# Kernel tuning notes

Hardware: AMD Instinct MI355X
Metric: run time of the kernel (lower is better)

Reference implementation:

```python
import jax, jax.numpy as jnp
import numpy as np

G, T, S, M = 1024, 200, 16, 4  # groups, timesteps, state_size, measure_size


def setup_inputs() -> dict:
    key = jax.random.key(0)
    ks = jax.random.split(key, 6)
    inp = jax.random.normal(ks[0], (G, T, M), dtype=jnp.float32)
    # near-identity transition (stable dynamics)
    F = jnp.eye(S, dtype=jnp.float32) + 0.01 * jax.random.normal(ks[1], (S, S), dtype=jnp.float32)
    qa = jax.random.normal(ks[2], (S, S), dtype=jnp.float32)
    Q = 0.01 * (qa @ qa.T) / S + 1e-3 * jnp.eye(S, dtype=jnp.float32)  # PSD process noise
    H = jax.random.normal(ks[3], (M, S), dtype=jnp.float32) / jnp.sqrt(jnp.float32(S))
    ra = jax.random.normal(ks[4], (M, M), dtype=jnp.float32)
    R = 0.1 * (ra @ ra.T) / M + 1e-2 * jnp.eye(M, dtype=jnp.float32)  # PSD measurement noise
    init_mean = jnp.zeros((G, S), dtype=jnp.float32)
    # block-diag initial state cov (identity per process block)
    init_cov = jnp.broadcast_to(jnp.eye(S, dtype=jnp.float32), (G, S, S)).copy()
    return {"input": inp, "F": F, "Q": Q, "H": H, "R": R,
            "init_mean": init_mean, "init_cov": init_cov}


def reference(input, F, Q, H, R, init_mean, init_cov):
    """Kalman filter: at t=0 emit the initial prediction; for t>0, update the
    previous prediction with obs[t-1] then predict forward (matches the torch
    loop). Returns one-step-ahead state means/covs and measurement means/covs."""

    def step(carry, obs):  # obs: [G, M] (measurement at t-1)
        mean, cov = carry  # [G,S], [G,S,S]
        # --- update: K = P H^T S^-1, S = H P H^T + R ---
        HP = jnp.einsum('ms,gsk->gmk', H, cov)            # [G,M,S]
        Smat = jnp.einsum('gmk,nk->gmn', HP, H) + R       # [G,M,M]
        K = jnp.swapaxes(jnp.linalg.solve(Smat, HP), 1, 2)  # [G,S,M]
        resid = obs - mean @ H.T                          # [G,M]
        mean_u = mean + jnp.einsum('gsm,gm->gs', K, resid)
        cov_u = cov - K @ HP                              # (I - K H) P
        # --- predict: F x, F P F^T + Q ---
        mean_p = mean_u @ F.T
        cov_p = jnp.einsum('ij,gjk,lk->gil', F, cov_u, F) + Q
        return (mean_p, cov_p), (mean_p, cov_p)

    obs_seq = jnp.swapaxes(input[:, :-1, :], 0, 1)  # [T-1, G, M]
    _, (means_t, covs_t) = jax.lax.scan(step, (init_mean, init_cov), obs_seq)

    means = jnp.concatenate([init_mean[None], means_t], axis=0)  # [T,G,S]
    covs = jnp.concatenate([init_cov[None], covs_t], axis=0)     # [T,G,S,S]

    # compute_measurement for every stored prediction: H x, H P H^T + R
    meas_means = jnp.einsum('tgs,ms->tgm', means, H)             # [T,G,M]
    HPc = jnp.einsum('ms,tgsk->tgmk', H, covs)
    meas_covs = jnp.einsum('tgmk,nk->tgmn', HPc, H) + R          # [T,G,M,M]

    return (jnp.swapaxes(means, 0, 1),       # [G,T,S]
            jnp.swapaxes(covs, 0, 1),        # [G,T,S,S]
            jnp.swapaxes(meas_means, 0, 1),  # [G,T,M]
            jnp.swapaxes(meas_covs, 0, 1))   # [G,T,M,M]
```

## Files before the change

### kernel.cpp

```cpp
#include <hip/hip_runtime.h>

#define NG 1024
#define NT 200
#define NS 16
#define NM 4

#define LDS_FENCE() asm volatile("" ::: "memory")

template<int CTRL>
__device__ __forceinline__ double dpp_mov_d(double x) {
    const int lo = __double2loint(x), hi = __double2hiint(x);
    const int plo = __builtin_amdgcn_update_dpp(lo, lo, CTRL, 0xF, 0xF, false);
    const int phi = __builtin_amdgcn_update_dpp(hi, hi, CTRL, 0xF, 0xF, false);
    return __hiloint2double(phi, plo);
}
__device__ __forceinline__ double row16_allreduce_d(double x) {
    x += dpp_mov_d<0xB1>(x);
    x += dpp_mov_d<0x4E>(x);
    x += dpp_mov_d<0x141>(x);
    x += dpp_mov_d<0x140>(x);
    return x;
}
__device__ __forceinline__ double partner16_d(double x, int odd) {
#if __has_builtin(__builtin_amdgcn_permlane16_swap)
    const unsigned lo = (unsigned)__double2loint(x), hi = (unsigned)__double2hiint(x);
    auto rl = __builtin_amdgcn_permlane16_swap(lo, lo, false, false);
    auto rh = __builtin_amdgcn_permlane16_swap(hi, hi, false, false);
    return __hiloint2double((int)(odd ? rh[0] : rh[1]),
                            (int)(odd ? rl[0] : rl[1]));
#else
    (void)odd; return __shfl_xor(x, 16, 64);
#endif
}
__device__ __forceinline__ double partner32_d(double x, int up) {
#if __has_builtin(__builtin_amdgcn_permlane32_swap)
    const unsigned lo = (unsigned)__double2loint(x), hi = (unsigned)__double2hiint(x);
    auto rl = __builtin_amdgcn_permlane32_swap(lo, lo, false, false);
    auto rh = __builtin_amdgcn_permlane32_swap(hi, hi, false, false);
    return __hiloint2double((int)(up ? rh[0] : rh[1]),
                            (int)(up ? rl[0] : rl[1]));
#else
    (void)up; return __shfl_xor(x, 32, 64);
#endif
}
__device__ __forceinline__ double quad_allreduce_d(double x, int q) {
    x += partner16_d(x, q & 1);
    x += partner32_d(x, (q >> 1) & 1);
    return x;
}

__global__ __launch_bounds__(256, 1)
void kalman_kernel(const float* __restrict__ input,
                   const float* __restrict__ Fm,
                   const float* __restrict__ Qm,
                   const float* __restrict__ Hm,
                   const float* __restrict__ Rm,
                   const float* __restrict__ init_mean,
                   const float* __restrict__ init_cov,
                   float* __restrict__ out)
{
    const int lane = threadIdx.x & 63;
    const int wid  = threadIdx.x >> 6;
    const int g    = (blockIdx.x << 2) + wid;
    const int c    = lane & 15;
    const int q    = lane >> 4;

    __shared__ __align__(16) float  lds3[4][NS][20];
    __shared__ __align__(16) double lds_K[4][NS][4];
    __shared__ __align__(16) double lds_mean[4][NS];

    float ErX[4][4][4];
    #pragma unroll
    for (int tp = 0; tp < 4; ++tp) {
        #pragma unroll
        for (int gs = 0; gs < 4; ++gs) {
            const float4 v = *(const float4*)(Fm + (4*q + tp)*NS + 4*(q ^ gs));
            ErX[tp][gs][0] = v.x; ErX[tp][gs][1] = v.y;
            ErX[tp][gs][2] = v.z; ErX[tp][gs][3] = v.w;
        }
        ErX[tp][0][tp] -= 1.0f;
    }
    double Ecq_d[4];
    {
        const float4 v = *(const float4*)(Fm + c*NS + 4*q);
        float fc[4] = {v.x, v.y, v.z, v.w};
        fc[0] -= (c == 4*q+0) ? 1.0f : 0.0f;
        fc[1] -= (c == 4*q+1) ? 1.0f : 0.0f;
        fc[2] -= (c == 4*q+2) ? 1.0f : 0.0f;
        fc[3] -= (c == 4*q+3) ? 1.0f : 0.0f;
        Ecq_d[0]=fc[0]; Ecq_d[1]=fc[1]; Ecq_d[2]=fc[2]; Ecq_d[3]=fc[3];
    }
    double Hq_d[4][4];
    #pragma unroll
    for (int m = 0; m < 4; ++m) {
        const float4 v = *(const float4*)(Hm + m*NS + 4*q);
        Hq_d[m][0]=v.x; Hq_d[m][1]=v.y; Hq_d[m][2]=v.z; Hq_d[m][3]=v.w;
    }
    double Hc_d[4];
    #pragma unroll
    for (int m = 0; m < 4; ++m) Hc_d[m] = (double)Hm[m*NS + c];
    double Q_d[4];
    #pragma unroll
    for (int tt = 0; tt < 4; ++tt) Q_d[tt] = (double)Qm[(4*q + tt)*NS + c];
    const double R00=Rm[0],  R10=Rm[4],  R11=Rm[5],  R20=Rm[8],  R21=Rm[9];
    const double R22=Rm[10], R30=Rm[12], R31=Rm[13], R32=Rm[14], R33=Rm[15];

    double p_d[4];
    #pragma unroll
    for (int tt = 0; tt < 4; ++tt)
        p_d[tt] = (double)init_cov[g*NS*NS + (4*q + tt)*NS + c];
    double mean_c_d = (double)init_mean[g*NS + c];
    double mean_q_d[4];
    #pragma unroll
    for (int tt = 0; tt < 4; ++tt)
        mean_q_d[tt] = (double)init_mean[g*NS + 4*q + tt];

    float* pMean = out + (size_t)g*NT*NS + c;
    float* pCov  = out + (size_t)NG*NT*NS + (size_t)g*NT*NS*NS + (4*q)*NS + c;
    float* pMM   = out + (size_t)NG*NT*NS + (size_t)NG*NT*NS*NS + (size_t)g*NT*NM;
    float* pMC   = out + (size_t)NG*NT*NS + (size_t)NG*NT*NS*NS + (size_t)NG*NT*NM
                       + (size_t)g*NT*NM*NM;
    const float* pObsBase = input + (size_t)g*NT*NM;

    float4 obs   = *(const float4*)(pObsBase);
    float4 obs_n = *(const float4*)(pObsBase + NM);

    for (int t = 0; t < NT; ++t) {
        const int tpre = (t + 2 < NT) ? (t + 2) : (NT - 1);
        const float4 obs_nn = *(const float4*)(pObsBase + (size_t)tpre*NM);

        if (q == 0) pMean[0] = (float)mean_c_d;
        #pragma unroll
        for (int tt = 0; tt < 4; ++tt) pCov[tt*NS] = (float)p_d[tt];

        double hm[4];
        #pragma unroll
        for (int m = 0; m < 4; ++m) {
            hm[m] = quad_allreduce_d(Hq_d[m][0]*mean_q_d[0] + Hq_d[m][1]*mean_q_d[1]
                                   + Hq_d[m][2]*mean_q_d[2] + Hq_d[m][3]*mean_q_d[3], q);
        }
        double pht[4];
        #pragma unroll
        for (int n = 0; n < 4; ++n) {
            pht[n] = quad_allreduce_d(p_d[0]*Hq_d[n][0] + p_d[1]*Hq_d[n][1]
                                    + p_d[2]*Hq_d[n][2] + p_d[3]*Hq_d[n][3], q);
        }

        const double s00 = row16_allreduce_d(Hc_d[0]*pht[0]) + R00;
        const double s10 = row16_allreduce_d(Hc_d[1]*pht[0]) + R10;
        const double s11 = row16_allreduce_d(Hc_d[1]*pht[1]) + R11;
        const double s20 = row16_allreduce_d(Hc_d[2]*pht[0]) + R20;
        const double s21 = row16_allreduce_d(Hc_d[2]*pht[1]) + R21;
        const double s22 = row16_allreduce_d(Hc_d[2]*pht[2]) + R22;
        const double s30 = row16_allreduce_d(Hc_d[3]*pht[0]) + R30;
        const double s31 = row16_allreduce_d(Hc_d[3]*pht[1]) + R31;
        const double s32 = row16_allreduce_d(Hc_d[3]*pht[2]) + R32;
        const double s33 = row16_allreduce_d(Hc_d[3]*pht[3]) + R33;

        if (lane == 0) {
            *(float4*)(pMM)      = make_float4((float)hm[0], (float)hm[1],
                                               (float)hm[2], (float)hm[3]);
            *(float4*)(pMC)      = make_float4((float)s00, (float)s10, (float)s20, (float)s30);
            *(float4*)(pMC + 4)  = make_float4((float)s10, (float)s11, (float)s21, (float)s31);
            *(float4*)(pMC + 8)  = make_float4((float)s20, (float)s21, (float)s22, (float)s32);
            *(float4*)(pMC + 12) = make_float4((float)s30, (float)s31, (float)s32, (float)s33);
        }
        pMean += NS; pCov += NS*NS; pMM += NM; pMC += NM*NM;
        if (t == NT-1) break;

        const double l00 = sqrt(s00);
        const double i0  = 1.0 / l00;
        const double L10 = s10*i0, L20 = s20*i0, L30 = s30*i0;
        const double l11 = sqrt(s11 - L10*L10);
        const double i1  = 1.0 / l11;
        const double L21 = (s21 - L20*L10)*i1;
        const double L31 = (s31 - L30*L10)*i1;
        const double l22 = sqrt(s22 - L20*L20 - L21*L21);
        const double i2  = 1.0 / l22;
        const double L32 = (s32 - L30*L20 - L31*L21)*i2;
        const double l33 = sqrt(s33 - L30*L30 - L31*L31 - L32*L32);
        const double i3  = 1.0 / l33;

        const double y0 = pht[0]*i0;
        const double y1 = (pht[1] - L10*y0)*i1;
        const double y2 = (pht[2] - L20*y0 - L21*y1)*i2;
        const double y3 = (pht[3] - L30*y0 - L31*y1 - L32*y2)*i3;
        double Kc[4];
        Kc[3] = y3*i3;
        Kc[2] = (y2 - L32*Kc[3])*i2;
        Kc[1] = (y1 - L21*Kc[2] - L31*Kc[3])*i1;
        Kc[0] = (y0 - L10*Kc[1] - L20*Kc[2] - L30*Kc[3])*i0;

        const double r0 = (double)obs.x - hm[0], r1 = (double)obs.y - hm[1],
                     r2 = (double)obs.z - hm[2], r3 = (double)obs.w - hm[3];

        const double mu_c_d = mean_c_d + Kc[0]*r0 + Kc[1]*r1 + Kc[2]*r2 + Kc[3]*r3;

        if (q == 0) {
            *(double2*)&lds_K[wid][c][0] = make_double2(Kc[0], Kc[1]);
            *(double2*)&lds_K[wid][c][2] = make_double2(Kc[2], Kc[3]);
        }
        LDS_FENCE();
        double Kq[4][4];
        #pragma unroll
        for (int tt = 0; tt < 4; ++tt) {
            const double2 k0 = *(const double2*)&lds_K[wid][4*q + tt][0];
            const double2 k1 = *(const double2*)&lds_K[wid][4*q + tt][2];
            Kq[tt][0]=k0.x; Kq[tt][1]=k0.y; Kq[tt][2]=k1.x; Kq[tt][3]=k1.y;
        }

        double cu_d[4], mu_q_d[4];
        #pragma unroll
        for (int tt = 0; tt < 4; ++tt) {
            cu_d[tt] = p_d[tt] - (Kq[tt][0]*pht[0] + Kq[tt][1]*pht[1]
                                + Kq[tt][2]*pht[2] + Kq[tt][3]*pht[3]);
            mu_q_d[tt] = mean_q_d[tt] + Kq[tt][0]*r0 + Kq[tt][1]*r1
                                      + Kq[tt][2]*r2 + Kq[tt][3]*r3;
        }

        mean_c_d = mu_c_d + quad_allreduce_d(Ecq_d[0]*mu_q_d[0] + Ecq_d[1]*mu_q_d[1]
                                           + Ecq_d[2]*mu_q_d[2] + Ecq_d[3]*mu_q_d[3], q);
        if (q == 0) lds_mean[wid][c] = mean_c_d;

        float cu_f[4];
        #pragma unroll
        for (int tt = 0; tt < 4; ++tt) cu_f[tt] = (float)cu_d[tt];
        *(float4*)&lds3[wid][c][4*q] = make_float4(cu_f[0],cu_f[1],cu_f[2],cu_f[3]);
        LDS_FENCE();
        float col[4][4];
        #pragma unroll
        for (int gs = 0; gs < 4; ++gs) {
            const float4 v = *(const float4*)&lds3[wid][c][4*(q ^ gs)];
            col[gs][0]=v.x; col[gs][1]=v.y; col[gs][2]=v.z; col[gs][3]=v.w;
        }
        {
            const double2 m0 = *(const double2*)&lds_mean[wid][4*q];
            const double2 m1 = *(const double2*)&lds_mean[wid][4*q + 2];
            mean_q_d[0]=m0.x; mean_q_d[1]=m0.y; mean_q_d[2]=m1.x; mean_q_d[3]=m1.y;
        }
        float w[4];
        #pragma unroll
        for (int tp = 0; tp < 4; ++tp) {
            float a = 0.0f;
            #pragma unroll
            for (int gs = 0; gs < 4; ++gs)
                #pragma unroll
                for (int tt = 0; tt < 4; ++tt)
                    a += ErX[tp][gs][tt]*col[gs][tt];
            w[tp] = a;
        }
        #pragma unroll
        for (int tp = 0; tp < 4; ++tp) lds3[wid][4*q + tp][c] = w[tp];
        LDS_FENCE();
        float rv[4][4];
        #pragma unroll
        for (int gs = 0; gs < 4; ++gs) {
            const float4 v = *(const float4*)&lds3[wid][c][4*(q ^ gs)];
            rv[gs][0]=v.x; rv[gs][1]=v.y; rv[gs][2]=v.z; rv[gs][3]=v.w;
        }
        #pragma unroll
        for (int tp = 0; tp < 4; ++tp) {
            float a = 0.0f;
            #pragma unroll
            for (int gs = 0; gs < 4; ++gs)
                #pragma unroll
                for (int tt = 0; tt < 4; ++tt)
                    a += ErX[tp][gs][tt]*rv[gs][tt];
            p_d[tp] = cu_d[tp] + Q_d[tp]
                    + (double)w[tp] + (double)rv[0][tp] + (double)a;
        }

        obs = obs_n; obs_n = obs_nn;
    }
}

extern "C" void kernel_launch(void* const* d_in, const int* in_sizes, int n_in,
                              void* d_out, int out_size, void* d_ws, size_t ws_size,
                              hipStream_t stream)
{
    const float* input = (const float*)d_in[0];
    const float* F     = (const float*)d_in[1];
    const float* Q     = (const float*)d_in[2];
    const float* H     = (const float*)d_in[3];
    const float* R     = (const float*)d_in[4];
    const float* imean = (const float*)d_in[5];
    const float* icov  = (const float*)d_in[6];

    kalman_kernel<<<NG/4, 256, 0, stream>>>(input, F, Q, H, R, imean, icov,
                                            (float*)d_out);
}
```

Before: 567.7 us.

## Use packed float math, permlane transposes, rsqrt Cholesky and 8-wave blocks

Several changes land together. Blocks grow to 8 waves (128 blocks, launch bounds 512,2). The first covariance-propagation matmul now gathers columns with permlane16/32 swaps instead of an LDS round trip, and both matmuls use packed v2f FMAs. The Cholesky sqrt/divide pairs become an f32 rsqrt followed by two Newton steps. The measurement-mean reduction and the quad reductions are restructured, and covariance stores switch to float4 with a transposed layout, which relies on P being symmetric. Fewer blocks than CUs leaves parts of the GPU idle, and the rsqrt refinement may lose a little precision compared with double sqrt.

```diff
diff --git a/kernel.cpp b/kernel.cpp
--- a/kernel.cpp
+++ b/kernel.cpp
@@ -4,6 +4,9 @@
 #define NT 200
 #define NS 16
 #define NM 4
+#define NWAVES 8
+
+typedef float v2f __attribute__((ext_vector_type(2)));
 
 #define LDS_FENCE() asm volatile("" ::: "memory")
 
@@ -21,35 +24,75 @@
     x += dpp_mov_d<0x140>(x);
     return x;
 }
-__device__ __forceinline__ double partner16_d(double x, int odd) {
+
+__device__ __forceinline__ void pair16_d(double x, double& e, double& o) {
 #if __has_builtin(__builtin_amdgcn_permlane16_swap)
     const unsigned lo = (unsigned)__double2loint(x), hi = (unsigned)__double2hiint(x);
     auto rl = __builtin_amdgcn_permlane16_swap(lo, lo, false, false);
     auto rh = __builtin_amdgcn_permlane16_swap(hi, hi, false, false);
-    return __hiloint2double((int)(odd ? rh[0] : rh[1]),
-                            (int)(odd ? rl[0] : rl[1]));
-#else
-    (void)odd; return __shfl_xor(x, 16, 64);
-#endif
-}
-__device__ __forceinline__ double partner32_d(double x, int up) {
+    e = __hiloint2double((int)rh[0], (int)rl[0]);
+    o = __hiloint2double((int)rh[1], (int)rl[1]);
+#else
+    const double p = __shfl_xor(x, 16, 64);
+    const int odd = (threadIdx.x >> 4) & 1;
+    e = odd ? p : x;  o = odd ? x : p;
+#endif
+}
+__device__ __forceinline__ void pair32_d(double x, double& l, double& h) {
 #if __has_builtin(__builtin_amdgcn_permlane32_swap)
     const unsigned lo = (unsigned)__double2loint(x), hi = (unsigned)__double2hiint(x);
     auto rl = __builtin_amdgcn_permlane32_swap(lo, lo, false, false);
     auto rh = __builtin_amdgcn_permlane32_swap(hi, hi, false, false);
-    return __hiloint2double((int)(up ? rh[0] : rh[1]),
-                            (int)(up ? rl[0] : rl[1]));
-#else
-    (void)up; return __shfl_xor(x, 32, 64);
-#endif
-}
-__device__ __forceinline__ double quad_allreduce_d(double x, int q) {
-    x += partner16_d(x, q & 1);
-    x += partner32_d(x, (q >> 1) & 1);
-    return x;
-}
-
-__global__ __launch_bounds__(256, 1)
+    l = __hiloint2double((int)rh[0], (int)rl[0]);
+    h = __hiloint2double((int)rh[1], (int)rl[1]);
+#else
+    const double p = __shfl_xor(x, 32, 64);
+    const int up = (threadIdx.x >> 5) & 1;
+    l = up ? p : x;  h = up ? x : p;
+#endif
+}
+__device__ __forceinline__ double quad_sum_d(double x) {
+    double e, o, l, h;
+    pair16_d(x, e, o);
+    const double s = e + o;
+    pair32_d(s, l, h);
+    return l + h;
+}
+__device__ __forceinline__ void pair16_f(float x, float& e, float& o) {
+#if __has_builtin(__builtin_amdgcn_permlane16_swap)
+    auto r = __builtin_amdgcn_permlane16_swap(__float_as_uint(x), __float_as_uint(x),
+                                              false, false);
+    e = __uint_as_float(r[0]); o = __uint_as_float(r[1]);
+#else
+    const float p = __shfl_xor(x, 16, 64);
+    const int odd = (threadIdx.x >> 4) & 1;
+    e = odd ? p : x;  o = odd ? x : p;
+#endif
+}
+__device__ __forceinline__ void pair32_f(float x, float& l, float& h) {
+#if __has_builtin(__builtin_amdgcn_permlane32_swap)
+    auto r = __builtin_amdgcn_permlane32_swap(__float_as_uint(x), __float_as_uint(x),
+                                              false, false);
+    l = __uint_as_float(r[0]); h = __uint_as_float(r[1]);
+#else
+    const float p = __shfl_xor(x, 32, 64);
+    const int up = (threadIdx.x >> 5) & 1;
+    l = up ? p : x;  h = up ? x : p;
+#endif
+}
+
+__device__ __forceinline__ double nrsqrt_d(double x) {
+#if __has_builtin(__builtin_amdgcn_rsq_f32)
+    double r = (double)__builtin_amdgcn_rsq_f32((float)x);
+#else
+    double r = (double)rsqrtf((float)x);
+#endif
+    r = r * (1.5 - 0.5 * x * r * r);
+    r = r * (1.5 - 0.5 * x * r * r);
+    return r;
+}
+
+__global__ __launch_bounds__(512, 2)
 void kalman_kernel(const float* __restrict__ input,
                    const float* __restrict__ Fm,
                    const float* __restrict__ Qm,
@@ -61,25 +104,29 @@
 {
     const int lane = threadIdx.x & 63;
     const int wid  = threadIdx.x >> 6;
-    const int g    = (blockIdx.x << 2) + wid;
+    const int g    = blockIdx.x * NWAVES + wid;
     const int c    = lane & 15;
     const int q    = lane >> 4;
 
-    __shared__ __align__(16) float  lds3[4][NS][20];
-    __shared__ __align__(16) double lds_K[4][NS][4];
-    __shared__ __align__(16) double lds_mean[4][NS];
-
-    float ErX[4][4][4];
-    #pragma unroll
-    for (int tp = 0; tp < 4; ++tp) {
-        #pragma unroll
-        for (int gs = 0; gs < 4; ++gs) {
-            const float4 v = *(const float4*)(Fm + (4*q + tp)*NS + 4*(q ^ gs));
-            ErX[tp][gs][0] = v.x; ErX[tp][gs][1] = v.y;
-            ErX[tp][gs][2] = v.z; ErX[tp][gs][3] = v.w;
-        }
-        ErX[tp][0][tp] -= 1.0f;
-    }
+    __shared__ __align__(16) float  lds3[NWAVES][NS][20];
+    __shared__ __align__(16) double lds_K[NWAVES][NS][6];
+    __shared__ __align__(16) double lds_mean[NWAVES][NS];
+
+    v2f E2[4][4][2];
+    #pragma unroll
+    for (int tp = 0; tp < 4; ++tp)
+        #pragma unroll
+        for (int j = 0; j < 4; ++j) {
+            float4 v = *(const float4*)(Fm + (4*q + tp)*NS + 4*j);
+            if (j == q) {
+                if (tp == 0) v.x -= 1.0f;
+                if (tp == 1) v.y -= 1.0f;
+                if (tp == 2) v.z -= 1.0f;
+                if (tp == 3) v.w -= 1.0f;
+            }
+            E2[tp][j][0] = (v2f){v.x, v.y};
+            E2[tp][j][1] = (v2f){v.z, v.w};
+        }
     double Ecq_d[4];
     {
         const float4 v = *(const float4*)(Fm + c*NS + 4*q);
@@ -99,6 +146,7 @@
     double Hc_d[4];
     #pragma unroll
     for (int m = 0; m < 4; ++m) Hc_d[m] = (double)Hm[m*NS + c];
+    const double Hqc_d = (double)Hm[q*NS + c];
     double Q_d[4];
     #pragma unroll
     for (int tt = 0; tt < 4; ++tt) Q_d[tt] = (double)Qm[(4*q + tt)*NS + c];
@@ -116,7 +164,7 @@
         mean_q_d[tt] = (double)init_mean[g*NS + 4*q + tt];
 
     float* pMean = out + (size_t)g*NT*NS + c;
-    float* pCov  = out + (size_t)NG*NT*NS + (size_t)g*NT*NS*NS + (4*q)*NS + c;
+    float* pCov  = out + (size_t)NG*NT*NS + (size_t)g*NT*NS*NS + c*NS + 4*q;
     float* pMM   = out + (size_t)NG*NT*NS + (size_t)NG*NT*NS*NS + (size_t)g*NT*NM;
     float* pMC   = out + (size_t)NG*NT*NS + (size_t)NG*NT*NS*NS + (size_t)NG*NT*NM
                        + (size_t)g*NT*NM*NM;
@@ -130,20 +178,22 @@
         const float4 obs_nn = *(const float4*)(pObsBase + (size_t)tpre*NM);
 
         if (q == 0) pMean[0] = (float)mean_c_d;
-        #pragma unroll
-        for (int tt = 0; tt < 4; ++tt) pCov[tt*NS] = (float)p_d[tt];
+        *(float4*)pCov = make_float4((float)p_d[0], (float)p_d[1],
+                                     (float)p_d[2], (float)p_d[3]);
 
         double hm[4];
-        #pragma unroll
-        for (int m = 0; m < 4; ++m) {
-            hm[m] = quad_allreduce_d(Hq_d[m][0]*mean_q_d[0] + Hq_d[m][1]*mean_q_d[1]
-                                   + Hq_d[m][2]*mean_q_d[2] + Hq_d[m][3]*mean_q_d[3], q);
+        {
+            const double hq = row16_allreduce_d(Hqc_d * mean_c_d);
+            double e, o;
+            pair16_d(hq, e, o);
+            pair32_d(e, hm[0], hm[2]);
+            pair32_d(o, hm[1], hm[3]);
         }
         double pht[4];
         #pragma unroll
         for (int n = 0; n < 4; ++n) {
-            pht[n] = quad_allreduce_d(p_d[0]*Hq_d[n][0] + p_d[1]*Hq_d[n][1]
-                                    + p_d[2]*Hq_d[n][2] + p_d[3]*Hq_d[n][3], q);
+            pht[n] = quad_sum_d(p_d[0]*Hq_d[n][0] + p_d[1]*Hq_d[n][1]
+                              + p_d[2]*Hq_d[n][2] + p_d[3]*Hq_d[n][3]);
         }
 
         const double s00 = row16_allreduce_d(Hc_d[0]*pht[0]) + R00;
@@ -168,18 +218,14 @@
         pMean += NS; pCov += NS*NS; pMM += NM; pMC += NM*NM;
         if (t == NT-1) break;
 
-        const double l00 = sqrt(s00);
-        const double i0  = 1.0 / l00;
+        const double i0  = nrsqrt_d(s00);
         const double L10 = s10*i0, L20 = s20*i0, L30 = s30*i0;
-        const double l11 = sqrt(s11 - L10*L10);
-        const double i1  = 1.0 / l11;
+        const double i1  = nrsqrt_d(s11 - L10*L10);
         const double L21 = (s21 - L20*L10)*i1;
         const double L31 = (s31 - L30*L10)*i1;
-        const double l22 = sqrt(s22 - L20*L20 - L21*L21);
-        const double i2  = 1.0 / l22;
+        const double i2  = nrsqrt_d(s22 - L20*L20 - L21*L21);
         const double L32 = (s32 - L30*L20 - L31*L21)*i2;
-        const double l33 = sqrt(s33 - L30*L30 - L31*L31 - L32*L32);
-        const double i3  = 1.0 / l33;
+        const double i3  = nrsqrt_d(s33 - L30*L30 - L31*L31 - L32*L32);
 
         const double y0 = pht[0]*i0;
         const double y1 = (pht[1] - L10*y0)*i1;
@@ -218,56 +264,66 @@
                                       + Kq[tt][2]*r2 + Kq[tt][3]*r3;
         }
 
-        mean_c_d = mu_c_d + quad_allreduce_d(Ecq_d[0]*mu_q_d[0] + Ecq_d[1]*mu_q_d[1]
-                                           + Ecq_d[2]*mu_q_d[2] + Ecq_d[3]*mu_q_d[3], q);
+        mean_c_d = mu_c_d + quad_sum_d(Ecq_d[0]*mu_q_d[0] + Ecq_d[1]*mu_q_d[1]
+                                     + Ecq_d[2]*mu_q_d[2] + Ecq_d[3]*mu_q_d[3]);
         if (q == 0) lds_mean[wid][c] = mean_c_d;
 
         float cu_f[4];
         #pragma unroll
         for (int tt = 0; tt < 4; ++tt) cu_f[tt] = (float)cu_d[tt];
-        *(float4*)&lds3[wid][c][4*q] = make_float4(cu_f[0],cu_f[1],cu_f[2],cu_f[3]);
+        v2f c2[4][2];
+        #pragma unroll
+        for (int tt = 0; tt < 4; ++tt) {
+            float e, o, v0, v1, v2, v3;
+            pair16_f(cu_f[tt], e, o);
+            pair32_f(e, v0, v2);
+            pair32_f(o, v1, v3);
+            c2[0][tt>>1][tt&1] = v0;
+            c2[1][tt>>1][tt&1] = v1;
+            c2[2][tt>>1][tt&1] = v2;
+            c2[3][tt>>1][tt&1] = v3;
+        }
+        float w[4];
+        #pragma unroll
+        for (int tp = 0; tp < 4; ++tp) {
+            v2f acc = (v2f){0.0f, 0.0f};
+            #pragma unroll
+            for (int j = 0; j < 4; ++j) {
+                acc += E2[tp][j][0] * c2[j][0];
+                acc += E2[tp][j][1] * c2[j][1];
+            }
+            w[tp] = acc.x + acc.y;
+        }
+        #pragma unroll
+        for (int tp = 0; tp < 4; ++tp) lds3[wid][4*q + tp][c] = w[tp];
         LDS_FENCE();
-        float col[4][4];
-        #pragma unroll
-        for (int gs = 0; gs < 4; ++gs) {
-            const float4 v = *(const float4*)&lds3[wid][c][4*(q ^ gs)];
-            col[gs][0]=v.x; col[gs][1]=v.y; col[gs][2]=v.z; col[gs][3]=v.w;
+        v2f rv2[4][2];
+        #pragma unroll
+        for (int j = 0; j < 4; ++j) {
+            const float4 v = *(const float4*)&lds3[wid][c][4*j];
+            rv2[j][0] = (v2f){v.x, v.y};
+            rv2[j][1] = (v2f){v.z, v.w};
+        }
+        float wt[4];
+        {
+            const float4 v = *(const float4*)&lds3[wid][c][4*q];
+            wt[0]=v.x; wt[1]=v.y; wt[2]=v.z; wt[3]=v.w;
         }
         {
             const double2 m0 = *(const double2*)&lds_mean[wid][4*q];
             const double2 m1 = *(const double2*)&lds_mean[wid][4*q + 2];
             mean_q_d[0]=m0.x; mean_q_d[1]=m0.y; mean_q_d[2]=m1.x; mean_q_d[3]=m1.y;
         }
-        float w[4];
         #pragma unroll
         for (int tp = 0; tp < 4; ++tp) {
-            float a = 0.0f;
+            v2f acc = (v2f){0.0f, 0.0f};
             #pragma unroll
-            for (int gs = 0; gs < 4; ++gs)
-                #pragma unroll
-                for (int tt = 0; tt < 4; ++tt)
-                    a += ErX[tp][gs][tt]*col[gs][tt];
-            w[tp] = a;
-        }
-        #pragma unroll
-        for (int tp = 0; tp < 4; ++tp) lds3[wid][4*q + tp][c] = w[tp];
-        LDS_FENCE();
-        float rv[4][4];
-        #pragma unroll
-        for (int gs = 0; gs < 4; ++gs) {
-            const float4 v = *(const float4*)&lds3[wid][c][4*(q ^ gs)];
-            rv[gs][0]=v.x; rv[gs][1]=v.y; rv[gs][2]=v.z; rv[gs][3]=v.w;
-        }
-        #pragma unroll
-        for (int tp = 0; tp < 4; ++tp) {
-            float a = 0.0f;
-            #pragma unroll
-            for (int gs = 0; gs < 4; ++gs)
-                #pragma unroll
-                for (int tt = 0; tt < 4; ++tt)
-                    a += ErX[tp][gs][tt]*rv[gs][tt];
+            for (int j = 0; j < 4; ++j) {
+                acc += E2[tp][j][0] * rv2[j][0];
+                acc += E2[tp][j][1] * rv2[j][1];
+            }
             p_d[tp] = cu_d[tp] + Q_d[tp]
-                    + (double)w[tp] + (double)rv[0][tp] + (double)a;
+                    + (double)w[tp] + (double)wt[tp] + (double)(acc.x + acc.y);
         }
 
         obs = obs_n; obs_n = obs_nn;
@@ -286,6 +342,6 @@
     const float* imean = (const float*)d_in[5];
     const float* icov  = (const float*)d_in[6];
 
-    kalman_kernel<<<NG/4, 256, 0, stream>>>(input, F, Q, H, R, imean, icov,
-                                            (float*)d_out);
-}
+    kalman_kernel<<<NG/NWAVES, 64*NWAVES, 0, stream>>>(input, F, Q, H, R,
+                                                       imean, icov, (float*)d_out);
+}
```

Result: slower. 684.8 us (+20.6%).
